# Optimization experiments

Hardware: AMD Instinct MI355X
Metric: run time of the kernel (lower is better)

The kernel has to match this reference:

```python
import jax, jax.numpy as jnp
import numpy as np

INPUT_DIM = 512
NUM_CLASSES = 1000


def setup_inputs() -> dict:
    key = jax.random.key(0)
    kx, kw, kb = jax.random.split(key, 3)
    x = jax.random.normal(kx, (16384, INPUT_DIM), dtype=jnp.float32)
    # Stacked per-class Linear(input_dim, 2) params: W [C, 2, D], b [C, 2]
    lim = 1.0 / np.sqrt(INPUT_DIM)
    W = jax.random.uniform(kw, (NUM_CLASSES, 2, INPUT_DIM), dtype=jnp.float32, minval=-lim, maxval=lim)
    b = jax.random.uniform(kb, (NUM_CLASSES, 2), dtype=jnp.float32, minval=-lim, maxval=lim)
    return {"x": x, "W": W, "b": b}


def reference(x, W, b):
    # logits[b, c, t] = x[b, :] @ W[c, t, :] + b[c, t]
    logits = jnp.einsum("bd,ctd->bct", x, W) + b[None, :, :]  # [B, C, 2]
    # LogSoftmax over the 2 logits per class (torch dim=1 of the [B,2] slice)
    return jax.nn.log_softmax(logits, axis=-1)
```

## Files before the change

kernel.cpp:

```cpp
#include <hip/hip_runtime.h>
#include <cstdint>
#include <cstddef>

typedef unsigned short u16;
typedef unsigned int u32;
typedef __bf16 bf16x8 __attribute__((ext_vector_type(8)));
typedef float f32x4 __attribute__((ext_vector_type(4)));
typedef float f32x2 __attribute__((ext_vector_type(2)));

#define M_TOT 16384
#define C_TOT 1000
#define N_PAD 1024
#define K_TOT 512
#define OUT_STRIDE 2000
#define BM 256
#define BN 256
#define BK 32
#define KSTEPS (K_TOT / BK)
#define MTILES (M_TOT / BM)
#define NTILES (N_PAD / BN)
#define NWG (MTILES * NTILES)

__device__ __forceinline__ u16 f2bf(float f) {
  u32 u = __float_as_uint(f);
  u = (u + 0x7FFFu + ((u >> 16) & 1u)) >> 16;
  return (u16)u;
}

__global__ __launch_bounds__(256) void cvt_kernel(const float* __restrict__ src,
                                                  u16* __restrict__ dst, int n8) {
  int i = blockIdx.x * blockDim.x + threadIdx.x;
  if (i >= n8) return;
  const float4* s = (const float4*)src;
  float4 a = s[2 * i], b = s[2 * i + 1];
  ushort4 r0, r1;
  r0.x = f2bf(a.x); r0.y = f2bf(a.y); r0.z = f2bf(a.z); r0.w = f2bf(a.w);
  r1.x = f2bf(b.x); r1.y = f2bf(b.y); r1.z = f2bf(b.z); r1.w = f2bf(b.w);
  ushort4* d = (ushort4*)dst;
  d[2 * i] = r0;
  d[2 * i + 1] = r1;
}

__global__ __launch_bounds__(256) void wdiff_kernel(const float* __restrict__ W,
                                                    const float* __restrict__ b,
                                                    u16* __restrict__ wd,
                                                    float* __restrict__ bd) {
  const int i = blockIdx.x * blockDim.x + threadIdx.x;
  const int c = i >> 6;
  const int seg = i & 63;
  if (c >= N_PAD) return;
  ushort4 r0 = {0, 0, 0, 0}, r1 = {0, 0, 0, 0};
  if (c < C_TOT) {
    const float4* w0 = (const float4*)(W + (size_t)(2 * c) * K_TOT) + seg * 2;
    const float4* w1 = (const float4*)(W + (size_t)(2 * c + 1) * K_TOT) + seg * 2;
    float4 a0 = w0[0], a1 = w0[1], c0 = w1[0], c1 = w1[1];
    r0.x = f2bf(a0.x - c0.x); r0.y = f2bf(a0.y - c0.y);
    r0.z = f2bf(a0.z - c0.z); r0.w = f2bf(a0.w - c0.w);
    r1.x = f2bf(a1.x - c1.x); r1.y = f2bf(a1.y - c1.y);
    r1.z = f2bf(a1.z - c1.z); r1.w = f2bf(a1.w - c1.w);
    if (seg == 0) bd[c] = b[2 * c] - b[2 * c + 1];
  } else if (seg == 0) {
    bd[c] = 0.0f;
  }
  ushort4* d = (ushort4*)(wd + (size_t)c * K_TOT);
  d[seg * 2] = r0;
  d[seg * 2 + 1] = r1;
}

__device__ __forceinline__ void gload_lds(const u16* g, u16* l) {
  __builtin_amdgcn_global_load_lds((const __attribute__((address_space(1))) u32*)g,
                                   (__attribute__((address_space(3))) u32*)l, 16, 0, 0);
}

__global__ __launch_bounds__(512, 2) void gemm_ls_kernel(const u16* __restrict__ A,
                                                         const u16* __restrict__ B,
                                                         const float* __restrict__ bdiff,
                                                         float* __restrict__ out) {
  __shared__ u16 As[2][BM * BK];
  __shared__ u16 Bs[2][BN * BK];

  const int tid = threadIdx.x;
  const int lane = tid & 63;
  const int w = tid >> 6;
  const int wm = w >> 2;
  const int wn = w & 3;

  const int bid = blockIdx.x;
  const int wg = (bid & 7) * (NWG / 8) + (bid >> 3);
  const int m0 = (wg >> 2) * BM;
  const int n0 = (wg & 3) * BN;

  const int srow = tid >> 2;
  const int sg = tid & 3;
  const u16* gA0 = A + (size_t)(m0 + srow) * K_TOT + sg * 8;
  const u16* gA1 = A + (size_t)(m0 + 128 + srow) * K_TOT + sg * 8;
  const u16* gB0 = B + (size_t)(n0 + srow) * K_TOT + sg * 8;
  const u16* gB1 = B + (size_t)(n0 + 128 + srow) * K_TOT + sg * 8;

  const int lo0 = tid * 8;
  const int lo1 = tid * 8 + 4096;

  f32x4 acc[8][4] = {};

  gload_lds(gA0, &As[0][lo0]);
  gload_lds(gA1, &As[0][lo1]);
  gload_lds(gB0, &Bs[0][lo0]);
  gload_lds(gB1, &Bs[0][lo1]);
  __syncthreads();

  const int ar = lane & 15;
  const int kq = (lane >> 4) * 16;

  int cur = 0;
  for (int kt = 0; kt < KSTEPS; ++kt) {
    if (kt < KSTEPS - 1) {
      const int ko = (kt + 1) * BK;
      const int nb = cur ^ 1;
      gload_lds(gA0 + ko, &As[nb][lo0]);
      gload_lds(gA1 + ko, &As[nb][lo1]);
      gload_lds(gB0 + ko, &Bs[nb][lo0]);
      gload_lds(gB1 + ko, &Bs[nb][lo1]);
    }

    bf16x8 af[8], bf[4];
#pragma unroll
    for (int mi = 0; mi < 8; ++mi) {
      const int row = wm * 128 + mi * 16 + ar;
      af[mi] = *(const bf16x8*)((const char*)&As[cur][0] + row * 64 + kq);
    }
#pragma unroll
    for (int ni = 0; ni < 4; ++ni) {
      const int row = wn * 64 + ni * 16 + ar;
      bf[ni] = *(const bf16x8*)((const char*)&Bs[cur][0] + row * 64 + kq);
    }
#pragma unroll
    for (int mi = 0; mi < 8; ++mi)
#pragma unroll
      for (int ni = 0; ni < 4; ++ni)
        acc[mi][ni] = __builtin_amdgcn_mfma_f32_16x16x32_bf16(af[mi], bf[ni], acc[mi][ni], 0, 0, 0);

    __syncthreads();
    cur ^= 1;
  }

  const int rbase = m0 + wm * 128 + (lane >> 4) * 4;
  const bool full = (n0 + BN <= C_TOT);

#pragma unroll
  for (int ni = 0; ni < 4; ++ni) {
    const int n = n0 + wn * 64 + ni * 16 + ar;
    if (full || n < C_TOT) {
      const float bd_r = bdiff[n];
#pragma unroll
      for (int mi = 0; mi < 8; ++mi) {
#pragma unroll
        for (int j = 0; j < 4; ++j) {
          const float d = acc[mi][ni][j] + bd_r;
          const float o0 = fminf(d, 0.0f) - __logf(1.0f + __expf(-fabsf(d)));
          const int row = rbase + mi * 16 + j;
          f32x2 v;
          v.x = o0;
          v.y = o0 - d;
          *(f32x2*)(out + (size_t)row * OUT_STRIDE + 2 * n) = v;
        }
      }
    }
  }
}

__global__ __launch_bounds__(256) void naive_kernel(const float* __restrict__ x,
                                                    const float* __restrict__ W,
                                                    const float* __restrict__ b,
                                                    float* __restrict__ out) {
  __shared__ float xs[K_TOT];
  const int row = blockIdx.x;
  for (int i = threadIdx.x; i < K_TOT; i += 256) xs[i] = x[(size_t)row * K_TOT + i];
  __syncthreads();
  for (int c = threadIdx.x; c < C_TOT; c += 256) {
    const float* w0 = W + (size_t)c * 1024;
    float l0 = b[c * 2], l1 = b[c * 2 + 1];
    for (int k = 0; k < K_TOT; ++k) {
      const float xv = xs[k];
      l0 += xv * w0[k];
      l1 += xv * w0[K_TOT + k];
    }
    const float d = l0 - l1;
    const float t = __logf(1.0f + __expf(-fabsf(d)));
    out[(size_t)row * OUT_STRIDE + c * 2]     = fminf(d, 0.0f) - t;
    out[(size_t)row * OUT_STRIDE + c * 2 + 1] = fminf(-d, 0.0f) - t;
  }
}

extern "C" void kernel_launch(void* const* d_in, const int* in_sizes, int n_in,
                              void* d_out, int out_size, void* d_ws, size_t ws_size,
                              hipStream_t stream) {
  const float* x = (const float*)d_in[0];
  const float* W = (const float*)d_in[1];
  const float* b = (const float*)d_in[2];
  float* out = (float*)d_out;

  const size_t nx = (size_t)M_TOT * K_TOT;
  const size_t nwd = (size_t)N_PAD * K_TOT;
  const size_t need = (nx + nwd) * sizeof(u16) + N_PAD * sizeof(float);

  if (ws_size < need) {
    naive_kernel<<<M_TOT, 256, 0, stream>>>(x, W, b, out);
    return;
  }

  u16* xb = (u16*)d_ws;
  u16* wd = xb + nx;
  float* bd = (float*)(wd + nwd);

  cvt_kernel<<<(int)(nx / 8 + 255) / 256, 256, 0, stream>>>(x, xb, (int)(nx / 8));
  wdiff_kernel<<<(N_PAD * 64) / 256, 256, 0, stream>>>(W, b, wd, bd);

  gemm_ls_kernel<<<NWG, 512, 0, stream>>>(xb, wd, bd, out);
}
```

Measured before the change: 59.29 us.

## Merge prep kernels and loop two 128-row tiles per GEMM block

Combines the x-to-bf16 conversion and weight-difference kernels into one launch, removing a kernel launch. The GEMM now uses 128x256 tiles with each workgroup processing two consecutive M tiles. It prefetches the next tile's first K-slice while the current tile's epilogue (log-softmax and stores) runs, so output writes overlap with loads. Accumulators shrink to 4x4, which lowers register pressure, but each workgroup re-reads the B tile once per M tile.

```diff
diff --git a/kernel.cpp b/kernel.cpp
--- a/kernel.cpp
+++ b/kernel.cpp
@@ -13,13 +13,12 @@
 #define N_PAD 1024
 #define K_TOT 512
 #define OUT_STRIDE 2000
-#define BM 256
+#define BM 128
 #define BN 256
 #define BK 32
 #define KSTEPS (K_TOT / BK)
-#define MTILES (M_TOT / BM)
-#define NTILES (N_PAD / BN)
-#define NWG (MTILES * NTILES)
+#define TILES_PER_BLOCK 2
+#define NWG 256
 
 __device__ __forceinline__ u16 f2bf(float f) {
   u32 u = __float_as_uint(f);
@@ -27,44 +26,43 @@
   return (u16)u;
 }
 
-__global__ __launch_bounds__(256) void cvt_kernel(const float* __restrict__ src,
-                                                  u16* __restrict__ dst, int n8) {
-  int i = blockIdx.x * blockDim.x + threadIdx.x;
-  if (i >= n8) return;
-  const float4* s = (const float4*)src;
-  float4 a = s[2 * i], b = s[2 * i + 1];
-  ushort4 r0, r1;
-  r0.x = f2bf(a.x); r0.y = f2bf(a.y); r0.z = f2bf(a.z); r0.w = f2bf(a.w);
-  r1.x = f2bf(b.x); r1.y = f2bf(b.y); r1.z = f2bf(b.z); r1.w = f2bf(b.w);
-  ushort4* d = (ushort4*)dst;
-  d[2 * i] = r0;
-  d[2 * i + 1] = r1;
-}
-
-__global__ __launch_bounds__(256) void wdiff_kernel(const float* __restrict__ W,
-                                                    const float* __restrict__ b,
-                                                    u16* __restrict__ wd,
-                                                    float* __restrict__ bd) {
-  const int i = blockIdx.x * blockDim.x + threadIdx.x;
-  const int c = i >> 6;
-  const int seg = i & 63;
-  if (c >= N_PAD) return;
-  ushort4 r0 = {0, 0, 0, 0}, r1 = {0, 0, 0, 0};
-  if (c < C_TOT) {
-    const float4* w0 = (const float4*)(W + (size_t)(2 * c) * K_TOT) + seg * 2;
-    const float4* w1 = (const float4*)(W + (size_t)(2 * c + 1) * K_TOT) + seg * 2;
-    float4 a0 = w0[0], a1 = w0[1], c0 = w1[0], c1 = w1[1];
-    r0.x = f2bf(a0.x - c0.x); r0.y = f2bf(a0.y - c0.y);
-    r0.z = f2bf(a0.z - c0.z); r0.w = f2bf(a0.w - c0.w);
-    r1.x = f2bf(a1.x - c1.x); r1.y = f2bf(a1.y - c1.y);
-    r1.z = f2bf(a1.z - c1.z); r1.w = f2bf(a1.w - c1.w);
-    if (seg == 0) bd[c] = b[2 * c] - b[2 * c + 1];
-  } else if (seg == 0) {
-    bd[c] = 0.0f;
-  }
-  ushort4* d = (ushort4*)(wd + (size_t)c * K_TOT);
-  d[seg * 2] = r0;
-  d[seg * 2 + 1] = r1;
+__global__ __launch_bounds__(256) void prep_kernel(const float* __restrict__ x,
+                                                   const float* __restrict__ W,
+                                                   const float* __restrict__ b,
+                                                   u16* __restrict__ xb,
+                                                   u16* __restrict__ wd,
+                                                   float* __restrict__ bd) {
+  if (blockIdx.x < 4096) {
+    const int i = blockIdx.x * 256 + threadIdx.x;
+    const float4* s = (const float4*)x;
+    float4 a = s[2 * i], c = s[2 * i + 1];
+    ushort4 r0, r1;
+    r0.x = f2bf(a.x); r0.y = f2bf(a.y); r0.z = f2bf(a.z); r0.w = f2bf(a.w);
+    r1.x = f2bf(c.x); r1.y = f2bf(c.y); r1.z = f2bf(c.z); r1.w = f2bf(c.w);
+    ushort4* d = (ushort4*)xb;
+    d[2 * i] = r0;
+    d[2 * i + 1] = r1;
+  } else {
+    const int i = (blockIdx.x - 4096) * 256 + threadIdx.x;
+    const int c = i >> 6;
+    const int seg = i & 63;
+    ushort4 r0 = {0, 0, 0, 0}, r1 = {0, 0, 0, 0};
+    if (c < C_TOT) {
+      const float4* w0 = (const float4*)(W + (size_t)(2 * c) * K_TOT) + seg * 2;
+      const float4* w1 = (const float4*)(W + (size_t)(2 * c + 1) * K_TOT) + seg * 2;
+      float4 a0 = w0[0], a1 = w0[1], c0 = w1[0], c1 = w1[1];
+      r0.x = f2bf(a0.x - c0.x); r0.y = f2bf(a0.y - c0.y);
+      r0.z = f2bf(a0.z - c0.z); r0.w = f2bf(a0.w - c0.w);
+      r1.x = f2bf(a1.x - c1.x); r1.y = f2bf(a1.y - c1.y);
+      r1.z = f2bf(a1.z - c1.z); r1.w = f2bf(a1.w - c1.w);
+      if (seg == 0) bd[c] = b[2 * c] - b[2 * c + 1];
+    } else if (seg == 0) {
+      bd[c] = 0.0f;
+    }
+    ushort4* d = (ushort4*)(wd + (size_t)c * K_TOT);
+    d[seg * 2] = r0;
+    d[seg * 2 + 1] = r1;
+  }
 }
 
 __device__ __forceinline__ void gload_lds(const u16* g, u16* l) {
@@ -87,81 +85,91 @@
 
   const int bid = blockIdx.x;
   const int wg = (bid & 7) * (NWG / 8) + (bid >> 3);
-  const int m0 = (wg >> 2) * BM;
+  const int m_base = (wg >> 2) * (BM * TILES_PER_BLOCK);
   const int n0 = (wg & 3) * BN;
 
   const int srow = tid >> 2;
   const int sg = tid & 3;
-  const u16* gA0 = A + (size_t)(m0 + srow) * K_TOT + sg * 8;
-  const u16* gA1 = A + (size_t)(m0 + 128 + srow) * K_TOT + sg * 8;
+  const u16* gA = A + (size_t)(m_base + srow) * K_TOT + sg * 8;
   const u16* gB0 = B + (size_t)(n0 + srow) * K_TOT + sg * 8;
-  const u16* gB1 = B + (size_t)(n0 + 128 + srow) * K_TOT + sg * 8;
-
-  const int lo0 = tid * 8;
-  const int lo1 = tid * 8 + 4096;
-
-  f32x4 acc[8][4] = {};
-
-  gload_lds(gA0, &As[0][lo0]);
-  gload_lds(gA1, &As[0][lo1]);
-  gload_lds(gB0, &Bs[0][lo0]);
-  gload_lds(gB1, &Bs[0][lo1]);
-  __syncthreads();
+  const u16* gB1 = gB0 + (size_t)128 * K_TOT;
+
+  const int loA = tid * 8;
+  const int loB0 = tid * 8;
+  const int loB1 = tid * 8 + 4096;
 
   const int ar = lane & 15;
   const int kq = (lane >> 4) * 16;
 
+  gload_lds(gA, &As[0][loA]);
+  gload_lds(gB0, &Bs[0][loB0]);
+  gload_lds(gB1, &Bs[0][loB1]);
+
   int cur = 0;
-  for (int kt = 0; kt < KSTEPS; ++kt) {
-    if (kt < KSTEPS - 1) {
-      const int ko = (kt + 1) * BK;
-      const int nb = cur ^ 1;
-      gload_lds(gA0 + ko, &As[nb][lo0]);
-      gload_lds(gA1 + ko, &As[nb][lo1]);
-      gload_lds(gB0 + ko, &Bs[nb][lo0]);
-      gload_lds(gB1 + ko, &Bs[nb][lo1]);
-    }
-
-    bf16x8 af[8], bf[4];
-#pragma unroll
-    for (int mi = 0; mi < 8; ++mi) {
-      const int row = wm * 128 + mi * 16 + ar;
-      af[mi] = *(const bf16x8*)((const char*)&As[cur][0] + row * 64 + kq);
-    }
+#pragma unroll
+  for (int t = 0; t < TILES_PER_BLOCK; ++t) {
+    const u16* gAt = gA + (size_t)t * BM * K_TOT;
+    f32x4 acc[4][4] = {};
+
+    __syncthreads();
+
+    for (int kt = 0; kt < KSTEPS; ++kt) {
+      if (kt < KSTEPS - 1) {
+        const int ko = (kt + 1) * BK;
+        const int nb = cur ^ 1;
+        gload_lds(gAt + ko, &As[nb][loA]);
+        gload_lds(gB0 + ko, &Bs[nb][loB0]);
+        gload_lds(gB1 + ko, &Bs[nb][loB1]);
+      }
+
+      bf16x8 af[4], bf[4];
+#pragma unroll
+      for (int mi = 0; mi < 4; ++mi) {
+        const int row = wm * 64 + mi * 16 + ar;
+        af[mi] = *(const bf16x8*)((const char*)&As[cur][0] + row * 64 + kq);
+      }
+#pragma unroll
+      for (int ni = 0; ni < 4; ++ni) {
+        const int row = wn * 64 + ni * 16 + ar;
+        bf[ni] = *(const bf16x8*)((const char*)&Bs[cur][0] + row * 64 + kq);
+      }
+#pragma unroll
+      for (int mi = 0; mi < 4; ++mi)
+#pragma unroll
+        for (int ni = 0; ni < 4; ++ni)
+          acc[mi][ni] = __builtin_amdgcn_mfma_f32_16x16x32_bf16(af[mi], bf[ni], acc[mi][ni], 0, 0, 0);
+
+      __syncthreads();
+      cur ^= 1;
+    }
+
+    if (t + 1 < TILES_PER_BLOCK) {
+      gload_lds(gAt + BM * K_TOT, &As[cur][loA]);
+      gload_lds(gB0, &Bs[cur][loB0]);
+      gload_lds(gB1, &Bs[cur][loB1]);
+    }
+
+    const int m0 = m_base + t * BM;
+    const int rbase = m0 + wm * 64 + (lane >> 4) * 4;
+    const bool full = (n0 + BN <= C_TOT);
+
 #pragma unroll
     for (int ni = 0; ni < 4; ++ni) {
-      const int row = wn * 64 + ni * 16 + ar;
-      bf[ni] = *(const bf16x8*)((const char*)&Bs[cur][0] + row * 64 + kq);
-    }
-#pragma unroll
-    for (int mi = 0; mi < 8; ++mi)
-#pragma unroll
-      for (int ni = 0; ni < 4; ++ni)
-        acc[mi][ni] = __builtin_amdgcn_mfma_f32_16x16x32_bf16(af[mi], bf[ni], acc[mi][ni], 0, 0, 0);
-
-    __syncthreads();
-    cur ^= 1;
-  }
-
-  const int rbase = m0 + wm * 128 + (lane >> 4) * 4;
-  const bool full = (n0 + BN <= C_TOT);
-
-#pragma unroll
-  for (int ni = 0; ni < 4; ++ni) {
-    const int n = n0 + wn * 64 + ni * 16 + ar;
-    if (full || n < C_TOT) {
-      const float bd_r = bdiff[n];
-#pragma unroll
-      for (int mi = 0; mi < 8; ++mi) {
-#pragma unroll
-        for (int j = 0; j < 4; ++j) {
-          const float d = acc[mi][ni][j] + bd_r;
-          const float o0 = fminf(d, 0.0f) - __logf(1.0f + __expf(-fabsf(d)));
-          const int row = rbase + mi * 16 + j;
-          f32x2 v;
-          v.x = o0;
-          v.y = o0 - d;
-          *(f32x2*)(out + (size_t)row * OUT_STRIDE + 2 * n) = v;
+      const int n = n0 + wn * 64 + ni * 16 + ar;
+      if (full || n < C_TOT) {
+        const float bd_r = bdiff[n];
+#pragma unroll
+        for (int mi = 0; mi < 4; ++mi) {
+#pragma unroll
+          for (int j = 0; j < 4; ++j) {
+            const float d = acc[mi][ni][j] + bd_r;
+            const float o0 = fminf(d, 0.0f) - __logf(1.0f + __expf(-fabsf(d)));
+            const int row = rbase + mi * 16 + j;
+            f32x2 v;
+            v.x = o0;
+            v.y = o0 - d;
+            *(f32x2*)(out + (size_t)row * OUT_STRIDE + 2 * n) = v;
+          }
         }
       }
     }
@@ -212,8 +220,6 @@
   u16* wd = xb + nx;
   float* bd = (float*)(wd + nwd);
 
-  cvt_kernel<<<(int)(nx / 8 + 255) / 256, 256, 0, stream>>>(x, xb, (int)(nx / 8));
-  wdiff_kernel<<<(N_PAD * 64) / 256, 256, 0, stream>>>(W, b, wd, bd);
-
+  prep_kernel<<<4096 + 256, 256, 0, stream>>>(x, W, b, xb, wd, bd);
   gemm_ls_kernel<<<NWG, 512, 0, stream>>>(xb, wd, bd, out);
 }
```

Result: faster. 57.88 us (-2.4%).

## Fuse x bf16 conversion into GEMM and stream pre-swizzled weights from global

Applied to the files above, without the earlier changes.

Drops the separate x-to-bf16 conversion kernel. The GEMM now loads fp32 x directly, converts it with packed cvt instructions and stores it into an XOR-swizzled LDS tile covering the full K range. The weight-difference kernel writes B in an MFMA fragment-ready layout, so each wave reads its B fragments straight from global memory into registers with double buffering. Tiles become 32 rows by 256 columns across 2048 workgroups of 256 threads. This removes a full pass over x and the workspace round trip. In exchange, every M-tile re-reads B from L2, and the mfma-to-load ratio per tile is lower.

```diff
diff --git a/kernel.cpp b/kernel.cpp
--- a/kernel.cpp
+++ b/kernel.cpp
@@ -7,19 +7,15 @@
 typedef __bf16 bf16x8 __attribute__((ext_vector_type(8)));
 typedef float f32x4 __attribute__((ext_vector_type(4)));
 typedef float f32x2 __attribute__((ext_vector_type(2)));
+typedef u32 u32x4 __attribute__((ext_vector_type(4)));
 
 #define M_TOT 16384
 #define C_TOT 1000
 #define N_PAD 1024
 #define K_TOT 512
 #define OUT_STRIDE 2000
-#define BM 256
-#define BN 256
-#define BK 32
-#define KSTEPS (K_TOT / BK)
-#define MTILES (M_TOT / BM)
-#define NTILES (N_PAD / BN)
-#define NWG (MTILES * NTILES)
+#define NT 16
+#define NWG 2048
 
 __device__ __forceinline__ u16 f2bf(float f) {
   u32 u = __float_as_uint(f);
@@ -27,28 +23,19 @@
   return (u16)u;
 }
 
-__global__ __launch_bounds__(256) void cvt_kernel(const float* __restrict__ src,
-                                                  u16* __restrict__ dst, int n8) {
-  int i = blockIdx.x * blockDim.x + threadIdx.x;
-  if (i >= n8) return;
-  const float4* s = (const float4*)src;
-  float4 a = s[2 * i], b = s[2 * i + 1];
-  ushort4 r0, r1;
-  r0.x = f2bf(a.x); r0.y = f2bf(a.y); r0.z = f2bf(a.z); r0.w = f2bf(a.w);
-  r1.x = f2bf(b.x); r1.y = f2bf(b.y); r1.z = f2bf(b.z); r1.w = f2bf(b.w);
-  ushort4* d = (ushort4*)dst;
-  d[2 * i] = r0;
-  d[2 * i + 1] = r1;
+__device__ __forceinline__ u32 cvtpk(float lo, float hi) {
+  u32 d;
+  asm("v_cvt_pk_bf16_f32 %0, %1, %2" : "=v"(d) : "v"(lo), "v"(hi));
+  return d;
 }
 
-__global__ __launch_bounds__(256) void wdiff_kernel(const float* __restrict__ W,
+__global__ __launch_bounds__(256) void wprep_kernel(const float* __restrict__ W,
                                                     const float* __restrict__ b,
                                                     u16* __restrict__ wd,
                                                     float* __restrict__ bd) {
-  const int i = blockIdx.x * blockDim.x + threadIdx.x;
+  const int i = blockIdx.x * 256 + threadIdx.x;
   const int c = i >> 6;
   const int seg = i & 63;
-  if (c >= N_PAD) return;
   ushort4 r0 = {0, 0, 0, 0}, r1 = {0, 0, 0, 0};
   if (c < C_TOT) {
     const float4* w0 = (const float4*)(W + (size_t)(2 * c) * K_TOT) + seg * 2;
@@ -62,106 +49,103 @@
   } else if (seg == 0) {
     bd[c] = 0.0f;
   }
-  ushort4* d = (ushort4*)(wd + (size_t)c * K_TOT);
-  d[seg * 2] = r0;
-  d[seg * 2 + 1] = r1;
+  const size_t idx = ((size_t)(c >> 4) * 16 + (seg >> 2)) * 512 +
+                     ((size_t)(c & 15) + (seg & 3) * 16) * 8;
+  *(ushort4*)(wd + idx) = r0;
+  *(ushort4*)(wd + idx + 4) = r1;
 }
 
-__device__ __forceinline__ void gload_lds(const u16* g, u16* l) {
-  __builtin_amdgcn_global_load_lds((const __attribute__((address_space(1))) u32*)g,
-                                   (__attribute__((address_space(3))) u32*)l, 16, 0, 0);
-}
-
-__global__ __launch_bounds__(512, 2) void gemm_ls_kernel(const u16* __restrict__ A,
-                                                         const u16* __restrict__ B,
+__global__ __launch_bounds__(256, 4) void gemm_ls_kernel(const float* __restrict__ Af,
+                                                         const u16* __restrict__ B2,
                                                          const float* __restrict__ bdiff,
                                                          float* __restrict__ out) {
-  __shared__ u16 As[2][BM * BK];
-  __shared__ u16 Bs[2][BN * BK];
+  __shared__ u16 Alds[32 * 512];
 
   const int tid = threadIdx.x;
   const int lane = tid & 63;
   const int w = tid >> 6;
-  const int wm = w >> 2;
-  const int wn = w & 3;
+  const int lrow = lane & 15;
+  const int lhi = lane >> 4;
 
   const int bid = blockIdx.x;
   const int wg = (bid & 7) * (NWG / 8) + (bid >> 3);
-  const int m0 = (wg >> 2) * BM;
-  const int n0 = (wg & 3) * BN;
+  const int m0 = (wg >> 2) * 32;
+  const int n0w = (wg & 3) * 256 + w * 64;
+  const int nf0 = n0w >> 4;
 
-  const int srow = tid >> 2;
-  const int sg = tid & 3;
-  const u16* gA0 = A + (size_t)(m0 + srow) * K_TOT + sg * 8;
-  const u16* gA1 = A + (size_t)(m0 + 128 + srow) * K_TOT + sg * 8;
-  const u16* gB0 = B + (size_t)(n0 + srow) * K_TOT + sg * 8;
-  const u16* gB1 = B + (size_t)(n0 + 128 + srow) * K_TOT + sg * 8;
+  float bd[4];
+  int ncol[4];
+#pragma unroll
+  for (int f = 0; f < 4; ++f) {
+    ncol[f] = n0w + f * 16 + lrow;
+    bd[f] = bdiff[ncol[f]];
+  }
 
-  const int lo0 = tid * 8;
-  const int lo1 = tid * 8 + 4096;
+  bf16x8 bfr[2][4];
+#pragma unroll
+  for (int f = 0; f < 4; ++f)
+    bfr[0][f] = *(const bf16x8*)(B2 + ((size_t)(nf0 + f) * 16 + 0) * 512 + lane * 8);
 
-  f32x4 acc[8][4] = {};
-
-  gload_lds(gA0, &As[0][lo0]);
-  gload_lds(gA1, &As[0][lo1]);
-  gload_lds(gB0, &Bs[0][lo0]);
-  gload_lds(gB1, &Bs[0][lo1]);
+#pragma unroll
+  for (int i = 0; i < 8; ++i) {
+    const int G = i * 256 + tid;
+    const int row = G >> 6, slot = G & 63;
+    const int g = slot ^ (row & 7);
+    const f32x4* src = (const f32x4*)(Af + (size_t)(m0 + row) * K_TOT + g * 8);
+    f32x4 a = src[0], c = src[1];
+    u32x4 wv;
+    wv.x = cvtpk(a.x, a.y);
+    wv.y = cvtpk(a.z, a.w);
+    wv.z = cvtpk(c.x, c.y);
+    wv.w = cvtpk(c.z, c.w);
+    *(u32x4*)(&Alds[(size_t)row * 512 + slot * 8]) = wv;
+  }
   __syncthreads();
 
-  const int ar = lane & 15;
-  const int kq = (lane >> 4) * 16;
+  f32x4 acc[2][4] = {};
+  const int abase0 = lrow * 1024;
+  const int abase1 = (16 + lrow) * 1024;
+  const int akey = lrow & 7;
 
-  int cur = 0;
-  for (int kt = 0; kt < KSTEPS; ++kt) {
-    if (kt < KSTEPS - 1) {
-      const int ko = (kt + 1) * BK;
-      const int nb = cur ^ 1;
-      gload_lds(gA0 + ko, &As[nb][lo0]);
-      gload_lds(gA1 + ko, &As[nb][lo1]);
-      gload_lds(gB0 + ko, &Bs[nb][lo0]);
-      gload_lds(gB1 + ko, &Bs[nb][lo1]);
-    }
+#define STEPK(T)                                                               \
+  do {                                                                         \
+    if ((T) < NT - 1) {                                                        \
+      _Pragma("unroll") for (int f = 0; f < 4; ++f)                            \
+          bfr[((T) + 1) & 1][f] = *(const bf16x8*)(                            \
+              B2 + ((size_t)(nf0 + f) * 16 + (T) + 1) * 512 + lane * 8);       \
+    }                                                                          \
+    const int s0 = (((((T) << 2) | lhi)) ^ akey) << 4;                         \
+    bf16x8 a0 = *(const bf16x8*)((const char*)Alds + abase0 + s0);             \
+    bf16x8 a1 = *(const bf16x8*)((const char*)Alds + abase1 + s0);             \
+    _Pragma("unroll") for (int f = 0; f < 4; ++f) {                            \
+      acc[0][f] = __builtin_amdgcn_mfma_f32_16x16x32_bf16(a0, bfr[(T) & 1][f], \
+                                                          acc[0][f], 0, 0, 0); \
+      acc[1][f] = __builtin_amdgcn_mfma_f32_16x16x32_bf16(a1, bfr[(T) & 1][f], \
+                                                          acc[1][f], 0, 0, 0); \
+    }                                                                          \
+  } while (0)
 
-    bf16x8 af[8], bf[4];
-#pragma unroll
-    for (int mi = 0; mi < 8; ++mi) {
-      const int row = wm * 128 + mi * 16 + ar;
-      af[mi] = *(const bf16x8*)((const char*)&As[cur][0] + row * 64 + kq);
-    }
-#pragma unroll
-    for (int ni = 0; ni < 4; ++ni) {
-      const int row = wn * 64 + ni * 16 + ar;
-      bf[ni] = *(const bf16x8*)((const char*)&Bs[cur][0] + row * 64 + kq);
-    }
-#pragma unroll
-    for (int mi = 0; mi < 8; ++mi)
-#pragma unroll
-      for (int ni = 0; ni < 4; ++ni)
-        acc[mi][ni] = __builtin_amdgcn_mfma_f32_16x16x32_bf16(af[mi], bf[ni], acc[mi][ni], 0, 0, 0);
-
-    __syncthreads();
-    cur ^= 1;
-  }
-
-  const int rbase = m0 + wm * 128 + (lane >> 4) * 4;
-  const bool full = (n0 + BN <= C_TOT);
+  STEPK(0);  STEPK(1);  STEPK(2);  STEPK(3);
+  STEPK(4);  STEPK(5);  STEPK(6);  STEPK(7);
+  STEPK(8);  STEPK(9);  STEPK(10); STEPK(11);
+  STEPK(12); STEPK(13); STEPK(14); STEPK(15);
+#undef STEPK
 
 #pragma unroll
-  for (int ni = 0; ni < 4; ++ni) {
-    const int n = n0 + wn * 64 + ni * 16 + ar;
-    if (full || n < C_TOT) {
-      const float bd_r = bdiff[n];
+  for (int f = 0; f < 4; ++f) {
+    if (ncol[f] < C_TOT) {
+      const float bd_r = bd[f];
 #pragma unroll
-      for (int mi = 0; mi < 8; ++mi) {
+      for (int mf = 0; mf < 2; ++mf) {
 #pragma unroll
         for (int j = 0; j < 4; ++j) {
-          const float d = acc[mi][ni][j] + bd_r;
+          const float d = acc[mf][f][j] + bd_r;
           const float o0 = fminf(d, 0.0f) - __logf(1.0f + __expf(-fabsf(d)));
-          const int row = rbase + mi * 16 + j;
+          const int row = m0 + mf * 16 + lhi * 4 + j;
           f32x2 v;
           v.x = o0;
           v.y = o0 - d;
-          *(f32x2*)(out + (size_t)row * OUT_STRIDE + 2 * n) = v;
+          *(f32x2*)(out + (size_t)row * OUT_STRIDE + 2 * ncol[f]) = v;
         }
       }
     }
@@ -199,21 +183,17 @@
   const float* b = (const float*)d_in[2];
   float* out = (float*)d_out;
 
-  const size_t nx = (size_t)M_TOT * K_TOT;
   const size_t nwd = (size_t)N_PAD * K_TOT;
-  const size_t need = (nx + nwd) * sizeof(u16) + N_PAD * sizeof(float);
+  const size_t need = nwd * sizeof(u16) + N_PAD * sizeof(float);
 
   if (ws_size < need) {
     naive_kernel<<<M_TOT, 256, 0, stream>>>(x, W, b, out);
     return;
   }
 
-  u16* xb = (u16*)d_ws;
-  u16* wd = xb + nx;
+  u16* wd = (u16*)d_ws;
   float* bd = (float*)(wd + nwd);
 
-  cvt_kernel<<<(int)(nx / 8 + 255) / 256, 256, 0, stream>>>(x, xb, (int)(nx / 8));
-  wdiff_kernel<<<(N_PAD * 64) / 256, 256, 0, stream>>>(W, b, wd, bd);
-
-  gemm_ls_kernel<<<NWG, 512, 0, stream>>>(xb, wd, bd, out);
+  wprep_kernel<<<256, 256, 0, stream>>>(W, b, wd, bd);
+  gemm_ls_kernel<<<NWG, 256, 0, stream>>>(x, wd, bd, out);
 }
```

Result: slower. 62.72 us (+5.8%).
